# Performance work log

Hardware: AMD Instinct MI355X
Metric: run time of the kernel (lower is better)

Reference implementation:

```python
import jax, jax.numpy as jnp
import numpy as np

K = 3      # kernel size (fixed by 18 = 2*K*K offset channels)
PAD = 1
EPS = 1e-5 # BatchNorm eps


def setup_inputs() -> dict:
    key = jax.random.key(0)
    ks = jax.random.split(key, 4)
    B, Cin, Cout, H, W = 8, 64, 64, 96, 96
    x = jax.random.normal(ks[0], (B, Cin, H, W), jnp.float32)
    # small offset-conv weights so predicted offsets stay within a few pixels
    w_off = jax.random.normal(ks[1], (2 * K * K, Cin, K, K), jnp.float32) * 0.02
    b_off = jnp.zeros((2 * K * K,), jnp.float32)
    w_def = jax.random.normal(ks[2], (Cout, Cin, K, K), jnp.float32) * (1.0 / np.sqrt(Cin * K * K))
    b_def = jnp.zeros((Cout,), jnp.float32)
    gamma = jnp.ones((Cout,), jnp.float32)
    beta = jnp.zeros((Cout,), jnp.float32)
    return dict(x=x, w_off=w_off, b_off=b_off, w_def=w_def, b_def=b_def, gamma=gamma, beta=beta)


def _deform_sample(x, offset):
    """Bilinear-sample x at deformed kernel tap locations.
    x: (B,C,H,W); offset: (B,2*K*K,H,W) with (dy,dx) pairs per tap, row-major.
    Returns (B,C,K*K,H,W). Out-of-bounds samples are zero (torchvision semantics).
    """
    B, C, H, W = x.shape
    off = offset.reshape(B, K * K, 2, H, W)
    dy, dx = off[:, :, 0], off[:, :, 1]              # (B,9,H,W)
    ky = (jnp.arange(K * K) // K).astype(x.dtype)    # tap row index
    kx = (jnp.arange(K * K) % K).astype(x.dtype)     # tap col index
    base_y = jnp.arange(H, dtype=x.dtype)[:, None] - PAD   # (H,1)
    base_x = jnp.arange(W, dtype=x.dtype)[None, :] - PAD   # (1,W)
    py = dy + ky[None, :, None, None] + base_y[None, None]  # (B,9,H,W)
    px = dx + kx[None, :, None, None] + base_x[None, None]
    y0 = jnp.floor(py)
    x0 = jnp.floor(px)
    wy1 = py - y0
    wx1 = px - x0
    wy0 = 1.0 - wy1
    wx0 = 1.0 - wx1
    xflat = x.reshape(B, C, H * W)
    acc = jnp.zeros((B, C, K * K * H * W), x.dtype)
    corners = [(y0, x0, wy0 * wx0), (y0, x0 + 1.0, wy0 * wx1),
               (y0 + 1.0, x0, wy1 * wx0), (y0 + 1.0, x0 + 1.0, wy1 * wx1)]
    for yc, xc, wc in corners:
        valid = (yc >= 0) & (yc <= H - 1) & (xc >= 0) & (xc <= W - 1)
        iy = jnp.clip(yc, 0, H - 1).astype(jnp.int32)
        ix = jnp.clip(xc, 0, W - 1).astype(jnp.int32)
        idx = (iy * W + ix).reshape(B, 1, K * K * H * W)
        v = jnp.take_along_axis(xflat, idx, axis=2)          # (B,C,9HW) gather
        w = jnp.where(valid, wc, 0.0).reshape(B, 1, K * K * H * W)
        acc = acc + v * w
    return acc.reshape(B, C, K * K, H, W)


def reference(x, w_off, b_off, w_def, b_def, gamma, beta):
    # 1) offset-predicting conv
    offset = jax.lax.conv_general_dilated(
        x, w_off, window_strides=(1, 1), padding=((PAD, PAD), (PAD, PAD)),
        dimension_numbers=("NCHW", "OIHW", "NCHW")) + b_off[None, :, None, None]
    # 2) deformable conv: bilinear gather then per-pixel contraction over (C, taps)
    sampled = _deform_sample(x, offset)                      # (B,C,9,H,W)
    Cout = w_def.shape[0]
    y = jnp.einsum("bckhw,ock->bohw", sampled, w_def.reshape(Cout, -1, K * K))
    y = y + b_def[None, :, None, None]
    # 3) BatchNorm2d (training mode: batch statistics) + ReLU
    mean = y.mean(axis=(0, 2, 3))
    var = y.var(axis=(0, 2, 3))
    y = (y - mean[None, :, None, None]) * jax.lax.rsqrt(var[None, :, None, None] + EPS)
    y = gamma[None, :, None, None] * y + beta[None, :, None, None]
    return jax.nn.relu(y)
```

## Files before the change

### kernel.cpp

```cpp
#include <hip/hip_runtime.h>
#include <hip/hip_bf16.h>
#include <stdint.h>

static constexpr int NBATCH = 8;
static constexpr int Cin  = 64;
static constexpr int Cout = 64;
static constexpr int H = 96, W = 96;
static constexpr int HW   = H * W;
static constexpr int NPIX = NBATCH * HW;
static constexpr int NBLK = NPIX / 64;
static constexpr int BLK_PER_BATCH = HW / 64;
static constexpr float EPS = 1e-5f;

typedef short  bf16x8 __attribute__((ext_vector_type(8)));
typedef float  f32x4  __attribute__((ext_vector_type(4)));

__device__ inline uint16_t f2bf(float f) {
    __hip_bfloat16 h = __float2bfloat16(f);
    return *reinterpret_cast<uint16_t*>(&h);
}
__device__ inline float bf2f(uint16_t u) {
    union { uint32_t i; float f; } z;
    z.i = ((uint32_t)u) << 16;
    return z.f;
}

__global__ void repack(const float* __restrict__ w_off,
                       const float* __restrict__ w_def,
                       uint16_t* __restrict__ woffPack,
                       uint16_t* __restrict__ wdefPack) {
    int t0 = blockIdx.x * blockDim.x + threadIdx.x;
    int stride = gridDim.x * blockDim.x;
    for (int i = t0; i < 72 * 32 * 8; i += stride) {
        int e = i & 7;
        int n = (i >> 3) & 31;
        int sg = i >> 8;
        int k = sg * 8 + e;
        int tap = k >> 6, c = k & 63;
        woffPack[i] = (n < 18) ? f2bf(w_off[(n * Cin + c) * 9 + tap]) : (uint16_t)0;
    }
    for (int i = t0; i < 72 * 64 * 8; i += stride) {
        int e = i & 7;
        int n = (i >> 3) & 63;
        int sg = i >> 9;
        int k = sg * 8 + e;
        int tap = k >> 6, c = k & 63;
        wdefPack[i] = f2bf(w_def[(n * Cin + c) * 9 + tap]);
    }
}

__global__ __launch_bounds__(256) void transpose_x(const float* __restrict__ x,
                                                   uint16_t* __restrict__ xT) {
    int t = blockIdx.x * 256 + threadIdx.x;
    int pix  = t >> 1;
    int half = t & 1;
    int b = pix / HW, rem = pix % HW;
    const float* xb = x + (size_t)(b * Cin) * HW + rem + (size_t)(half * 32) * HW;
    uint16_t* o = xT + (size_t)pix * 64 + half * 32;
#pragma unroll
    for (int cg = 0; cg < 4; ++cg) {
        bf16x8 v;
#pragma unroll
        for (int e = 0; e < 8; ++e) v[e] = (short)f2bf(xb[(cg * 8 + e) * HW]);
        *reinterpret_cast<bf16x8*>(o + cg * 8) = v;
    }
}

__global__ __launch_bounds__(512, 4) void fused_deform(
        const uint16_t* __restrict__ xT,
        const uint16_t* __restrict__ woffPack,
        const uint16_t* __restrict__ wdefPack,
        const float* __restrict__ b_off,
        float* __restrict__ y,
        float* __restrict__ partial) {
    __shared__ __attribute__((aligned(16))) char smem[73728];
    __shared__ float offs[64 * 18];
    __shared__ float s_red[128];
    short* As   = (short*)smem;
    float* osum = (float*)smem;
    float* red  = (float*)smem;

    int tid  = threadIdx.x;
    int lane = tid & 63;
    int wv   = tid >> 6;
    int l15  = lane & 15;
    int lg   = lane >> 4;

    int wgid  = (blockIdx.x & 7) * BLK_PER_BATCH + (blockIdx.x >> 3);
    int gpix0 = wgid * 64;
    int b     = gpix0 / HW;
    int rem0  = gpix0 % HW;
    const uint16_t* xTb = xT + (size_t)b * HW * 64;

    int pr   = (wv << 3) + (lane >> 3);
    int e8   = lane & 7;
    int slot = e8 ^ (pr & 7);
    int remP = rem0 + pr;
    int hP   = remP / W, wP = remP % W;

#pragma unroll
    for (int tap = 0; tap < 9; ++tap) {
        int yy = hP + tap / 3 - 1;
        int xx = wP + tap % 3 - 1;
        bf16x8 v = (bf16x8){0, 0, 0, 0, 0, 0, 0, 0};
        if (yy >= 0 && yy < H && xx >= 0 && xx < W)
            v = *reinterpret_cast<const bf16x8*>(xTb + (yy * W + xx) * 64 + e8 * 8);
        *reinterpret_cast<bf16x8*>(&As[((tap * 64 + pr) * 8 + slot) * 8]) = v;
    }
    __syncthreads();

    {
        int wj = wv & 1;
        int kq = wv >> 1;
        int sbeg = (kq < 2) ? kq * 5 : 2 + kq * 4;
        int send = (kq < 2) ? sbeg + 5 : sbeg + 4;
        f32x4 oacc[4];
#pragma unroll
        for (int m = 0; m < 4; ++m) oacc[m] = (f32x4){0.f, 0.f, 0.f, 0.f};
        for (int s = sbeg; s < send; ++s) {
            int sg = s * 4 + lg;
            bf16x8 bb = *reinterpret_cast<const bf16x8*>(
                woffPack + (sg * 32 + wj * 16 + l15) * 8);
#pragma unroll
            for (int m = 0; m < 4; ++m) {
                bf16x8 a = *reinterpret_cast<const bf16x8*>(
                    &As[(((sg >> 3) * 64 + m * 16 + l15) * 8 + ((sg & 7) ^ (l15 & 7))) * 8]);
                oacc[m] = __builtin_amdgcn_mfma_f32_16x16x32_bf16(a, bb, oacc[m], 0, 0, 0);
            }
        }
        __syncthreads();
#pragma unroll
        for (int m = 0; m < 4; ++m)
#pragma unroll
            for (int r = 0; r < 4; ++r)
                osum[(kq * 64 + m * 16 + lg * 4 + r) * 34 + wj * 16 + l15] = oacc[m][r];
        __syncthreads();
        for (int i = tid; i < 64 * 18; i += 512) {
            int rr = i / 18, o = i - rr * 18;
            offs[i] = osum[rr * 34 + o] + osum[(64 + rr) * 34 + o]
                    + osum[(128 + rr) * 34 + o] + osum[(192 + rr) * 34 + o] + b_off[o];
        }
        if (tid < 128) s_red[tid] = 0.f;
        __syncthreads();
    }

    float hm1 = (float)(hP - 1), wm1 = (float)(wP - 1);
#pragma unroll
    for (int tap = 0; tap < 9; ++tap) {
        float dy = offs[pr * 18 + 2 * tap];
        float dx = offs[pr * 18 + 2 * tap + 1];
        float py = dy + (float)(tap / 3) + hm1;
        float px = dx + (float)(tap % 3) + wm1;
        float y0f = floorf(py), x0f = floorf(px);
        float wy1 = py - y0f, wx1 = px - x0f;
        float wy0 = 1.f - wy1, wx0 = 1.f - wx1;
        int iy0 = (int)y0f, ix0 = (int)x0f;
        int iy1 = iy0 + 1,  ix1 = ix0 + 1;
        bool vy0 = (iy0 >= 0) && (iy0 < H), vy1 = (iy1 >= 0) && (iy1 < H);
        bool vx0 = (ix0 >= 0) && (ix0 < W), vx1 = (ix1 >= 0) && (ix1 < W);
        float w00 = (vy0 && vx0) ? wy0 * wx0 : 0.f;
        float w01 = (vy0 && vx1) ? wy0 * wx1 : 0.f;
        float w10 = (vy1 && vx0) ? wy1 * wx0 : 0.f;
        float w11 = (vy1 && vx1) ? wy1 * wx1 : 0.f;
        int cy0 = min(max(iy0, 0), H - 1), cy1 = min(max(iy1, 0), H - 1);
        int cx0 = min(max(ix0, 0), W - 1), cx1 = min(max(ix1, 0), W - 1);
        const uint16_t* basep = xTb + e8 * 8;
        bf16x8 v00 = *reinterpret_cast<const bf16x8*>(basep + (cy0 * W + cx0) * 64);
        bf16x8 v01 = *reinterpret_cast<const bf16x8*>(basep + (cy0 * W + cx1) * 64);
        bf16x8 v10 = *reinterpret_cast<const bf16x8*>(basep + (cy1 * W + cx0) * 64);
        bf16x8 v11 = *reinterpret_cast<const bf16x8*>(basep + (cy1 * W + cx1) * 64);
        bf16x8 outv;
#pragma unroll
        for (int e = 0; e < 8; ++e) {
            float s = w00 * bf2f((uint16_t)v00[e]) + w01 * bf2f((uint16_t)v01[e])
                    + w10 * bf2f((uint16_t)v10[e]) + w11 * bf2f((uint16_t)v11[e]);
            outv[e] = (short)f2bf(s);
        }
        *reinterpret_cast<bf16x8*>(&As[((tap * 64 + pr) * 8 + slot) * 8]) = outv;
    }
    __syncthreads();

    {
        int nf = wv & 3;
        int kh = wv >> 2;
        f32x4 acc[4];
#pragma unroll
        for (int m = 0; m < 4; ++m) acc[m] = (f32x4){0.f, 0.f, 0.f, 0.f};
#pragma unroll
        for (int s = 0; s < 9; ++s) {
            int sg = (kh * 9 + s) * 4 + lg;
            bf16x8 bb = *reinterpret_cast<const bf16x8*>(
                wdefPack + (sg * 64 + nf * 16 + l15) * 8);
#pragma unroll
            for (int m = 0; m < 4; ++m) {
                bf16x8 a = *reinterpret_cast<const bf16x8*>(
                    &As[(((sg >> 3) * 64 + m * 16 + l15) * 8 + ((sg & 7) ^ (l15 & 7))) * 8]);
                acc[m] = __builtin_amdgcn_mfma_f32_16x16x32_bf16(a, bb, acc[m], 0, 0, 0);
            }
        }
        __syncthreads();
#pragma unroll
        for (int m = 0; m < 4; ++m)
#pragma unroll
            for (int r = 0; r < 4; ++r)
                red[(kh * 64 + m * 16 + lg * 4 + r) * 66 + nf * 16 + l15] = acc[m][r];
        __syncthreads();

        int c  = lane;
        int rg = wv;
        f32x4 v0, v1;
        float s = 0.f, q = 0.f;
#pragma unroll
        for (int k2 = 0; k2 < 8; ++k2) {
            int r = rg * 8 + k2;
            float v = red[r * 66 + c] + red[(64 + r) * 66 + c];
            if (k2 < 4) v0[k2] = v; else v1[k2 - 4] = v;
            s += v; q += v * v;
        }
        float* yp = y + ((size_t)b * Cout + c) * HW + rem0 + rg * 8;
        *reinterpret_cast<f32x4*>(yp)     = v0;
        *reinterpret_cast<f32x4*>(yp + 4) = v1;
        atomicAdd(&s_red[c], s);
        atomicAdd(&s_red[64 + c], q);
    }
    __syncthreads();
    if (tid < 128) partial[(size_t)wgid * 128 + tid] = s_red[tid];
}

__global__ __launch_bounds__(256) void bn_reduce1(const float* __restrict__ partial,
                                                  float* __restrict__ partial2) {
    __shared__ float red[256];
    int ch = threadIdx.x & 127;
    int g  = threadIdx.x >> 7;
    float s = 0.f;
#pragma unroll
    for (int r = 0; r < 8; ++r)
        s += partial[(size_t)(blockIdx.x * 16 + g * 8 + r) * 128 + ch];
    red[threadIdx.x] = s;
    __syncthreads();
    if (g == 0)
        partial2[(size_t)blockIdx.x * 128 + ch] = red[ch] + red[128 + ch];
}

__global__ void bn_stats2(const float* __restrict__ partial2,
                          const float* __restrict__ gamma,
                          const float* __restrict__ beta,
                          float* __restrict__ stats) {
    __shared__ float red[256];
    int ch = threadIdx.x & 127;
    int g  = threadIdx.x >> 7;
    float s = 0.f;
    for (int i = 0; i < 36; ++i)
        s += partial2[(size_t)(g * 36 + i) * 128 + ch];
    red[threadIdx.x] = s;
    __syncthreads();
    if (threadIdx.x < 64) {
        int c = threadIdx.x;
        float sum = red[c] + red[128 + c];
        float sq  = red[64 + c] + red[192 + c];
        float mean = sum / (float)NPIX;
        float var  = sq / (float)NPIX - mean * mean;
        float v    = var + EPS;
        float inv  = rsqrtf(v);
        inv = inv * (1.5f - 0.5f * v * inv * inv);
        float sc = gamma[c] * inv;
        stats[c]      = sc;
        stats[64 + c] = beta[c] - mean * sc;
    }
}

__global__ __launch_bounds__(256) void bn_apply(float* __restrict__ y,
                                                const float* __restrict__ stats) {
    int t = blockIdx.x * blockDim.x + threadIdx.x;
    int e = t * 4;
    int ch = (e / HW) % Cout;
    float sc = stats[ch];
    float sh = stats[64 + ch];
    float4 v = *reinterpret_cast<float4*>(y + e);
    v.x = fmaxf(v.x * sc + sh, 0.f);
    v.y = fmaxf(v.y * sc + sh, 0.f);
    v.z = fmaxf(v.z * sc + sh, 0.f);
    v.w = fmaxf(v.w * sc + sh, 0.f);
    *reinterpret_cast<float4*>(y + e) = v;
}

extern "C" void kernel_launch(void* const* d_in, const int* in_sizes, int n_in,
                              void* d_out, int out_size, void* d_ws, size_t ws_size,
                              hipStream_t stream) {
    const float* x     = (const float*)d_in[0];
    const float* w_off = (const float*)d_in[1];
    const float* b_off = (const float*)d_in[2];
    const float* w_def = (const float*)d_in[3];
    const float* gamma = (const float*)d_in[5];
    const float* beta  = (const float*)d_in[6];
    float* out = (float*)d_out;
    char*  ws  = (char*)d_ws;

    uint16_t* xT       = (uint16_t*)ws;
    uint16_t* woffPack = (uint16_t*)(ws + 9437184);
    uint16_t* wdefPack = (uint16_t*)(ws + 9474048);
    float*    partial  = (float*)(ws + 9547776);
    float*    partial2 = (float*)(ws + 10137600);
    float*    stats    = (float*)(ws + 10174464);

    repack<<<64, 256, 0, stream>>>(w_off, w_def, woffPack, wdefPack);
    transpose_x<<<NPIX * 2 / 256, 256, 0, stream>>>(x, xT);
    fused_deform<<<NBLK, 512, 0, stream>>>(xT, woffPack, wdefPack, b_off,
                                           out, partial);
    bn_reduce1<<<72, 256, 0, stream>>>(partial, partial2);
    bn_stats2<<<1, 256, 0, stream>>>(partial2, gamma, beta, stats);
    bn_apply<<<(NPIX * Cout / 4) / 256, 256, 0, stream>>>(out, stats);
}
```

Before: 69.26 us.

## Halve pixel tile to 32 and read offset-conv operands directly from global

Shrinks the per-workgroup pixel tile from 64 to 32, which halves LDS use and doubles the workgroup count, and raises the launch-bounds occupancy hint from 4 to 8. The offset conv no longer stages the 9-tap im2col in LDS. It loads A fragments straight from the transposed input in global memory with bounds masking, which removes one staging pass and one barrier. Bilinear sampling is re-split so the two halves of the block handle different tap ranges, and the BN partial reduction is resized for the doubled number of partials. The cost is more redundant global loads, since neighbouring tiles overlap more and the weight fragments are fetched once per smaller tile.

```diff
diff --git a/kernel.cpp b/kernel.cpp
--- a/kernel.cpp
+++ b/kernel.cpp
@@ -8,8 +8,9 @@
 static constexpr int H = 96, W = 96;
 static constexpr int HW   = H * W;
 static constexpr int NPIX = NBATCH * HW;
-static constexpr int NBLK = NPIX / 64;
-static constexpr int BLK_PER_BATCH = HW / 64;
+static constexpr int NTILE = 32;
+static constexpr int NBLK = NPIX / NTILE;
+static constexpr int BLK_PER_BATCH = HW / NTILE;
 static constexpr float EPS = 1e-5f;
 
 typedef short  bf16x8 __attribute__((ext_vector_type(8)));
@@ -66,15 +67,15 @@
     }
 }
 
-__global__ __launch_bounds__(512, 4) void fused_deform(
+__global__ __launch_bounds__(512, 8) void fused_deform(
         const uint16_t* __restrict__ xT,
         const uint16_t* __restrict__ woffPack,
         const uint16_t* __restrict__ wdefPack,
         const float* __restrict__ b_off,
         float* __restrict__ y,
         float* __restrict__ partial) {
-    __shared__ __attribute__((aligned(16))) char smem[73728];
-    __shared__ float offs[64 * 18];
+    __shared__ __attribute__((aligned(16))) char smem[36864];
+    __shared__ float offs[NTILE * 18];
     __shared__ float s_red[128];
     short* As   = (short*)smem;
     float* osum = (float*)smem;
@@ -87,139 +88,135 @@
     int lg   = lane >> 4;
 
     int wgid  = (blockIdx.x & 7) * BLK_PER_BATCH + (blockIdx.x >> 3);
-    int gpix0 = wgid * 64;
+    int gpix0 = wgid * NTILE;
     int b     = gpix0 / HW;
     int rem0  = gpix0 % HW;
+    int h0    = rem0 / W;
+    int w0    = rem0 % W;
     const uint16_t* xTb = xT + (size_t)b * HW * 64;
 
-    int pr   = (wv << 3) + (lane >> 3);
-    int e8   = lane & 7;
-    int slot = e8 ^ (pr & 7);
-    int remP = rem0 + pr;
-    int hP   = remP / W, wP = remP % W;
-
-#pragma unroll
-    for (int tap = 0; tap < 9; ++tap) {
-        int yy = hP + tap / 3 - 1;
-        int xx = wP + tap % 3 - 1;
-        bf16x8 v = (bf16x8){0, 0, 0, 0, 0, 0, 0, 0};
-        if (yy >= 0 && yy < H && xx >= 0 && xx < W)
-            v = *reinterpret_cast<const bf16x8*>(xTb + (yy * W + xx) * 64 + e8 * 8);
-        *reinterpret_cast<bf16x8*>(&As[((tap * 64 + pr) * 8 + slot) * 8]) = v;
-    }
-    __syncthreads();
+    if (tid < 128) s_red[tid] = 0.f;
 
     {
         int wj = wv & 1;
         int kq = wv >> 1;
         int sbeg = (kq < 2) ? kq * 5 : 2 + kq * 4;
         int send = (kq < 2) ? sbeg + 5 : sbeg + 4;
-        f32x4 oacc[4];
-#pragma unroll
-        for (int m = 0; m < 4; ++m) oacc[m] = (f32x4){0.f, 0.f, 0.f, 0.f};
+        f32x4 oacc[2];
+        oacc[0] = (f32x4){0.f, 0.f, 0.f, 0.f};
+        oacc[1] = (f32x4){0.f, 0.f, 0.f, 0.f};
         for (int s = sbeg; s < send; ++s) {
             int sg = s * 4 + lg;
+            int tap = sg >> 3, ch = sg & 7;
+            int ty = tap / 3, tx = tap % 3;
+            int yy = h0 + ty - 1;
             bf16x8 bb = *reinterpret_cast<const bf16x8*>(
                 woffPack + (sg * 32 + wj * 16 + l15) * 8);
 #pragma unroll
-            for (int m = 0; m < 4; ++m) {
+            for (int m = 0; m < 2; ++m) {
+                int xx = w0 + m * 16 + l15 + tx - 1;
+                bool ok = (yy >= 0) && (yy < H) && (xx >= 0) && (xx < W);
+                int cy = min(max(yy, 0), H - 1);
+                int cx = min(max(xx, 0), W - 1);
                 bf16x8 a = *reinterpret_cast<const bf16x8*>(
-                    &As[(((sg >> 3) * 64 + m * 16 + l15) * 8 + ((sg & 7) ^ (l15 & 7))) * 8]);
+                    xTb + (cy * W + cx) * 64 + ch * 8);
+                if (!ok) a = (bf16x8){0, 0, 0, 0, 0, 0, 0, 0};
                 oacc[m] = __builtin_amdgcn_mfma_f32_16x16x32_bf16(a, bb, oacc[m], 0, 0, 0);
             }
         }
+#pragma unroll
+        for (int m = 0; m < 2; ++m)
+#pragma unroll
+            for (int r = 0; r < 4; ++r)
+                osum[(kq * 32 + m * 16 + lg * 4 + r) * 34 + wj * 16 + l15] = oacc[m][r];
         __syncthreads();
-#pragma unroll
-        for (int m = 0; m < 4; ++m)
-#pragma unroll
-            for (int r = 0; r < 4; ++r)
-                osum[(kq * 64 + m * 16 + lg * 4 + r) * 34 + wj * 16 + l15] = oacc[m][r];
+        for (int i = tid; i < NTILE * 18; i += 512) {
+            int rr = i / 18, o = i - rr * 18;
+            offs[i] = osum[rr * 34 + o] + osum[(32 + rr) * 34 + o]
+                    + osum[(64 + rr) * 34 + o] + osum[(96 + rr) * 34 + o] + b_off[o];
+        }
         __syncthreads();
-        for (int i = tid; i < 64 * 18; i += 512) {
-            int rr = i / 18, o = i - rr * 18;
-            offs[i] = osum[rr * 34 + o] + osum[(64 + rr) * 34 + o]
-                    + osum[(128 + rr) * 34 + o] + osum[(192 + rr) * 34 + o] + b_off[o];
-        }
-        if (tid < 128) s_red[tid] = 0.f;
-        __syncthreads();
-    }
-
-    float hm1 = (float)(hP - 1), wm1 = (float)(wP - 1);
-#pragma unroll
-    for (int tap = 0; tap < 9; ++tap) {
-        float dy = offs[pr * 18 + 2 * tap];
-        float dx = offs[pr * 18 + 2 * tap + 1];
-        float py = dy + (float)(tap / 3) + hm1;
-        float px = dx + (float)(tap % 3) + wm1;
-        float y0f = floorf(py), x0f = floorf(px);
-        float wy1 = py - y0f, wx1 = px - x0f;
-        float wy0 = 1.f - wy1, wx0 = 1.f - wx1;
-        int iy0 = (int)y0f, ix0 = (int)x0f;
-        int iy1 = iy0 + 1,  ix1 = ix0 + 1;
-        bool vy0 = (iy0 >= 0) && (iy0 < H), vy1 = (iy1 >= 0) && (iy1 < H);
-        bool vx0 = (ix0 >= 0) && (ix0 < W), vx1 = (ix1 >= 0) && (ix1 < W);
-        float w00 = (vy0 && vx0) ? wy0 * wx0 : 0.f;
-        float w01 = (vy0 && vx1) ? wy0 * wx1 : 0.f;
-        float w10 = (vy1 && vx0) ? wy1 * wx0 : 0.f;
-        float w11 = (vy1 && vx1) ? wy1 * wx1 : 0.f;
-        int cy0 = min(max(iy0, 0), H - 1), cy1 = min(max(iy1, 0), H - 1);
-        int cx0 = min(max(ix0, 0), W - 1), cx1 = min(max(ix1, 0), W - 1);
-        const uint16_t* basep = xTb + e8 * 8;
-        bf16x8 v00 = *reinterpret_cast<const bf16x8*>(basep + (cy0 * W + cx0) * 64);
-        bf16x8 v01 = *reinterpret_cast<const bf16x8*>(basep + (cy0 * W + cx1) * 64);
-        bf16x8 v10 = *reinterpret_cast<const bf16x8*>(basep + (cy1 * W + cx0) * 64);
-        bf16x8 v11 = *reinterpret_cast<const bf16x8*>(basep + (cy1 * W + cx1) * 64);
-        bf16x8 outv;
-#pragma unroll
-        for (int e = 0; e < 8; ++e) {
-            float s = w00 * bf2f((uint16_t)v00[e]) + w01 * bf2f((uint16_t)v01[e])
-                    + w10 * bf2f((uint16_t)v10[e]) + w11 * bf2f((uint16_t)v11[e]);
-            outv[e] = (short)f2bf(s);
-        }
-        *reinterpret_cast<bf16x8*>(&As[((tap * 64 + pr) * 8 + slot) * 8]) = outv;
+    }
+
+    {
+        int e8 = tid & 7;
+        int pr = (tid >> 3) & 31;
+        int g  = tid >> 8;
+        int slot = e8 ^ (pr & 7);
+        float hm1 = (float)(h0 - 1), wm1 = (float)(w0 + pr - 1);
+        int tbeg = g ? 5 : 0, tend = g ? 9 : 5;
+        for (int tap = tbeg; tap < tend; ++tap) {
+            float dy = offs[pr * 18 + 2 * tap];
+            float dx = offs[pr * 18 + 2 * tap + 1];
+            float py = dy + (float)(tap / 3) + hm1;
+            float px = dx + (float)(tap % 3) + wm1;
+            float y0f = floorf(py), x0f = floorf(px);
+            float wy1 = py - y0f, wx1 = px - x0f;
+            float wy0 = 1.f - wy1, wx0 = 1.f - wx1;
+            int iy0 = (int)y0f, ix0 = (int)x0f;
+            int iy1 = iy0 + 1,  ix1 = ix0 + 1;
+            bool vy0 = (iy0 >= 0) && (iy0 < H), vy1 = (iy1 >= 0) && (iy1 < H);
+            bool vx0 = (ix0 >= 0) && (ix0 < W), vx1 = (ix1 >= 0) && (ix1 < W);
+            float w00 = (vy0 && vx0) ? wy0 * wx0 : 0.f;
+            float w01 = (vy0 && vx1) ? wy0 * wx1 : 0.f;
+            float w10 = (vy1 && vx0) ? wy1 * wx0 : 0.f;
+            float w11 = (vy1 && vx1) ? wy1 * wx1 : 0.f;
+            int cy0 = min(max(iy0, 0), H - 1), cy1 = min(max(iy1, 0), H - 1);
+            int cx0 = min(max(ix0, 0), W - 1), cx1 = min(max(ix1, 0), W - 1);
+            const uint16_t* basep = xTb + e8 * 8;
+            bf16x8 v00 = *reinterpret_cast<const bf16x8*>(basep + (cy0 * W + cx0) * 64);
+            bf16x8 v01 = *reinterpret_cast<const bf16x8*>(basep + (cy0 * W + cx1) * 64);
+            bf16x8 v10 = *reinterpret_cast<const bf16x8*>(basep + (cy1 * W + cx0) * 64);
+            bf16x8 v11 = *reinterpret_cast<const bf16x8*>(basep + (cy1 * W + cx1) * 64);
+            bf16x8 outv;
+#pragma unroll
+            for (int e = 0; e < 8; ++e) {
+                float s = w00 * bf2f((uint16_t)v00[e]) + w01 * bf2f((uint16_t)v01[e])
+                        + w10 * bf2f((uint16_t)v10[e]) + w11 * bf2f((uint16_t)v11[e]);
+                outv[e] = (short)f2bf(s);
+            }
+            *reinterpret_cast<bf16x8*>(&As[((tap * 32 + pr) * 8 + slot) * 8]) = outv;
+        }
     }
     __syncthreads();
 
     {
         int nf = wv & 3;
         int kh = wv >> 2;
-        f32x4 acc[4];
-#pragma unroll
-        for (int m = 0; m < 4; ++m) acc[m] = (f32x4){0.f, 0.f, 0.f, 0.f};
-#pragma unroll
+        f32x4 acc[2];
+        acc[0] = (f32x4){0.f, 0.f, 0.f, 0.f};
+        acc[1] = (f32x4){0.f, 0.f, 0.f, 0.f};
+#pragma unroll 3
         for (int s = 0; s < 9; ++s) {
             int sg = (kh * 9 + s) * 4 + lg;
             bf16x8 bb = *reinterpret_cast<const bf16x8*>(
                 wdefPack + (sg * 64 + nf * 16 + l15) * 8);
 #pragma unroll
-            for (int m = 0; m < 4; ++m) {
+            for (int m = 0; m < 2; ++m) {
                 bf16x8 a = *reinterpret_cast<const bf16x8*>(
-                    &As[(((sg >> 3) * 64 + m * 16 + l15) * 8 + ((sg & 7) ^ (l15 & 7))) * 8]);
+                    &As[(((sg >> 3) * 32 + m * 16 + l15) * 8 + ((sg & 7) ^ (l15 & 7))) * 8]);
                 acc[m] = __builtin_amdgcn_mfma_f32_16x16x32_bf16(a, bb, acc[m], 0, 0, 0);
             }
         }
         __syncthreads();
 #pragma unroll
-        for (int m = 0; m < 4; ++m)
+        for (int m = 0; m < 2; ++m)
 #pragma unroll
             for (int r = 0; r < 4; ++r)
-                red[(kh * 64 + m * 16 + lg * 4 + r) * 66 + nf * 16 + l15] = acc[m][r];
+                red[(kh * 32 + m * 16 + lg * 4 + r) * 66 + nf * 16 + l15] = acc[m][r];
         __syncthreads();
 
-        int c  = lane;
-        int rg = wv;
-        f32x4 v0, v1;
+        int c    = tid >> 3;
+        int pgrp = (tid & 7) * 4;
         float s = 0.f, q = 0.f;
-#pragma unroll
-        for (int k2 = 0; k2 < 8; ++k2) {
-            int r = rg * 8 + k2;
-            float v = red[r * 66 + c] + red[(64 + r) * 66 + c];
-            if (k2 < 4) v0[k2] = v; else v1[k2 - 4] = v;
-            s += v; q += v * v;
-        }
-        float* yp = y + ((size_t)b * Cout + c) * HW + rem0 + rg * 8;
-        *reinterpret_cast<f32x4*>(yp)     = v0;
-        *reinterpret_cast<f32x4*>(yp + 4) = v1;
+        f32x4 v;
+#pragma unroll
+        for (int i = 0; i < 4; ++i) {
+            int r = pgrp + i;
+            float val = red[r * 66 + c] + red[(32 + r) * 66 + c];
+            v[i] = val; s += val; q += val * val;
+        }
+        *reinterpret_cast<f32x4*>(y + ((size_t)b * Cout + c) * HW + rem0 + pgrp) = v;
         atomicAdd(&s_red[c], s);
         atomicAdd(&s_red[64 + c], q);
     }
@@ -234,8 +231,8 @@
     int g  = threadIdx.x >> 7;
     float s = 0.f;
 #pragma unroll
-    for (int r = 0; r < 8; ++r)
-        s += partial[(size_t)(blockIdx.x * 16 + g * 8 + r) * 128 + ch];
+    for (int r = 0; r < 16; ++r)
+        s += partial[(size_t)(blockIdx.x * 32 + g * 16 + r) * 128 + ch];
     red[threadIdx.x] = s;
     __syncthreads();
     if (g == 0)
@@ -300,8 +297,8 @@
     uint16_t* woffPack = (uint16_t*)(ws + 9437184);
     uint16_t* wdefPack = (uint16_t*)(ws + 9474048);
     float*    partial  = (float*)(ws + 9547776);
-    float*    partial2 = (float*)(ws + 10137600);
-    float*    stats    = (float*)(ws + 10174464);
+    float*    partial2 = (float*)(ws + 10727424);
+    float*    stats    = (float*)(ws + 10764288);
 
     repack<<<64, 256, 0, stream>>>(w_off, w_def, woffPack, wdefPack);
     transpose_x<<<NPIX * 2 / 256, 256, 0, stream>>>(x, xT);
```

Result: slower. 77.82 us (+12.3%).

## Stage im2col taps via global_load_lds and share bilinear setup across lanes

Applied to the files above, without the earlier changes.

The initial 3x3 neighbourhood load into LDS now uses direct global-to-LDS 16-byte loads, with out-of-bounds taps redirected to a zeroed scratch page written by the repack kernel. The swizzled slot is applied on the global source side so the LDS layout stays the same as before. In the deformable sampling stage, each of the 8 lanes that share a pixel computes the bilinear weights and indices for one tap, and the values are broadcast with shuffles, so the per-tap scalar math is no longer repeated across all 8 lanes. Tap 8 is still computed redundantly. The aim is to cut VGPR traffic and redundant ALU work, at the cost of 8 shuffles per tap and a dependence on the global_load_lds layout matching the previous LDS indexing.

```diff
diff --git a/kernel.cpp b/kernel.cpp
--- a/kernel.cpp
+++ b/kernel.cpp
@@ -24,13 +24,20 @@
     z.i = ((uint32_t)u) << 16;
     return z.f;
 }
+__device__ inline void gld_lds16(const void* g, void* l) {
+    __builtin_amdgcn_global_load_lds(
+        (const __attribute__((address_space(1))) void*)g,
+        (__attribute__((address_space(3))) void*)l, 16, 0, 0);
+}
 
 __global__ void repack(const float* __restrict__ w_off,
                        const float* __restrict__ w_def,
                        uint16_t* __restrict__ woffPack,
-                       uint16_t* __restrict__ wdefPack) {
+                       uint16_t* __restrict__ wdefPack,
+                       float* __restrict__ zeropage) {
     int t0 = blockIdx.x * blockDim.x + threadIdx.x;
     int stride = gridDim.x * blockDim.x;
+    if (t0 < 64) zeropage[t0] = 0.f;
     for (int i = t0; i < 72 * 32 * 8; i += stride) {
         int e = i & 7;
         int n = (i >> 3) & 31;
@@ -71,6 +78,7 @@
         const uint16_t* __restrict__ woffPack,
         const uint16_t* __restrict__ wdefPack,
         const float* __restrict__ b_off,
+        const float* __restrict__ zeropage,
         float* __restrict__ y,
         float* __restrict__ partial) {
     __shared__ __attribute__((aligned(16))) char smem[73728];
@@ -98,14 +106,18 @@
     int remP = rem0 + pr;
     int hP   = remP / W, wP = remP % W;
 
-#pragma unroll
-    for (int tap = 0; tap < 9; ++tap) {
-        int yy = hP + tap / 3 - 1;
-        int xx = wP + tap % 3 - 1;
-        bf16x8 v = (bf16x8){0, 0, 0, 0, 0, 0, 0, 0};
-        if (yy >= 0 && yy < H && xx >= 0 && xx < W)
-            v = *reinterpret_cast<const bf16x8*>(xTb + (yy * W + xx) * 64 + e8 * 8);
-        *reinterpret_cast<bf16x8*>(&As[((tap * 64 + pr) * 8 + slot) * 8]) = v;
+    {
+        const uint16_t* gsrc = xTb + slot * 8;
+        char* ldsbase = (char*)As + (size_t)wv * 1024;
+#pragma unroll
+        for (int tap = 0; tap < 9; ++tap) {
+            int yy = hP + tap / 3 - 1;
+            int xx = wP + tap % 3 - 1;
+            bool ok = (yy >= 0) && (yy < H) && (xx >= 0) && (xx < W);
+            const void* g = ok ? (const void*)(gsrc + (yy * W + xx) * 64)
+                               : (const void*)zeropage;
+            gld_lds16(g, ldsbase + tap * 8192);
+        }
     }
     __syncthreads();
 
@@ -144,39 +156,84 @@
         __syncthreads();
     }
 
-    float hm1 = (float)(hP - 1), wm1 = (float)(wP - 1);
-#pragma unroll
-    for (int tap = 0; tap < 9; ++tap) {
-        float dy = offs[pr * 18 + 2 * tap];
-        float dx = offs[pr * 18 + 2 * tap + 1];
-        float py = dy + (float)(tap / 3) + hm1;
-        float px = dx + (float)(tap % 3) + wm1;
-        float y0f = floorf(py), x0f = floorf(px);
-        float wy1 = py - y0f, wx1 = px - x0f;
-        float wy0 = 1.f - wy1, wx0 = 1.f - wx1;
-        int iy0 = (int)y0f, ix0 = (int)x0f;
-        int iy1 = iy0 + 1,  ix1 = ix0 + 1;
-        bool vy0 = (iy0 >= 0) && (iy0 < H), vy1 = (iy1 >= 0) && (iy1 < H);
-        bool vx0 = (ix0 >= 0) && (ix0 < W), vx1 = (ix1 >= 0) && (ix1 < W);
-        float w00 = (vy0 && vx0) ? wy0 * wx0 : 0.f;
-        float w01 = (vy0 && vx1) ? wy0 * wx1 : 0.f;
-        float w10 = (vy1 && vx0) ? wy1 * wx0 : 0.f;
-        float w11 = (vy1 && vx1) ? wy1 * wx1 : 0.f;
-        int cy0 = min(max(iy0, 0), H - 1), cy1 = min(max(iy1, 0), H - 1);
-        int cx0 = min(max(ix0, 0), W - 1), cx1 = min(max(ix1, 0), W - 1);
+    {
+        float hm1 = (float)(hP - 1), wm1 = (float)(wP - 1);
+        float w00a, w01a, w10a, w11a; int i00a, i01a, i10a, i11a;
+        {
+            int t = e8;
+            int ty = (t * 11) >> 5;
+            int tx = t - 3 * ty;
+            float dy = offs[pr * 18 + 2 * t];
+            float dx = offs[pr * 18 + 2 * t + 1];
+            float py = dy + (float)ty + hm1;
+            float px = dx + (float)tx + wm1;
+            float y0f = floorf(py), x0f = floorf(px);
+            float wy1 = py - y0f, wx1 = px - x0f;
+            float wy0 = 1.f - wy1, wx0 = 1.f - wx1;
+            int iy0 = (int)y0f, ix0 = (int)x0f;
+            int iy1 = iy0 + 1,  ix1 = ix0 + 1;
+            bool vy0 = (iy0 >= 0) && (iy0 < H), vy1 = (iy1 >= 0) && (iy1 < H);
+            bool vx0 = (ix0 >= 0) && (ix0 < W), vx1 = (ix1 >= 0) && (ix1 < W);
+            w00a = (vy0 && vx0) ? wy0 * wx0 : 0.f;
+            w01a = (vy0 && vx1) ? wy0 * wx1 : 0.f;
+            w10a = (vy1 && vx0) ? wy1 * wx0 : 0.f;
+            w11a = (vy1 && vx1) ? wy1 * wx1 : 0.f;
+            int cy0 = min(max(iy0, 0), H - 1), cy1 = min(max(iy1, 0), H - 1);
+            int cx0 = min(max(ix0, 0), W - 1), cx1 = min(max(ix1, 0), W - 1);
+            i00a = cy0 * W + cx0; i01a = cy0 * W + cx1;
+            i10a = cy1 * W + cx0; i11a = cy1 * W + cx1;
+        }
+        float w00b, w01b, w10b, w11b; int i00b, i01b, i10b, i11b;
+        {
+            float dy = offs[pr * 18 + 16];
+            float dx = offs[pr * 18 + 17];
+            float py = dy + 2.f + hm1;
+            float px = dx + 2.f + wm1;
+            float y0f = floorf(py), x0f = floorf(px);
+            float wy1 = py - y0f, wx1 = px - x0f;
+            float wy0 = 1.f - wy1, wx0 = 1.f - wx1;
+            int iy0 = (int)y0f, ix0 = (int)x0f;
+            int iy1 = iy0 + 1,  ix1 = ix0 + 1;
+            bool vy0 = (iy0 >= 0) && (iy0 < H), vy1 = (iy1 >= 0) && (iy1 < H);
+            bool vx0 = (ix0 >= 0) && (ix0 < W), vx1 = (ix1 >= 0) && (ix1 < W);
+            w00b = (vy0 && vx0) ? wy0 * wx0 : 0.f;
+            w01b = (vy0 && vx1) ? wy0 * wx1 : 0.f;
+            w10b = (vy1 && vx0) ? wy1 * wx0 : 0.f;
+            w11b = (vy1 && vx1) ? wy1 * wx1 : 0.f;
+            int cy0 = min(max(iy0, 0), H - 1), cy1 = min(max(iy1, 0), H - 1);
+            int cx0 = min(max(ix0, 0), W - 1), cx1 = min(max(ix1, 0), W - 1);
+            i00b = cy0 * W + cx0; i01b = cy0 * W + cx1;
+            i10b = cy1 * W + cx0; i11b = cy1 * W + cx1;
+        }
+
         const uint16_t* basep = xTb + e8 * 8;
-        bf16x8 v00 = *reinterpret_cast<const bf16x8*>(basep + (cy0 * W + cx0) * 64);
-        bf16x8 v01 = *reinterpret_cast<const bf16x8*>(basep + (cy0 * W + cx1) * 64);
-        bf16x8 v10 = *reinterpret_cast<const bf16x8*>(basep + (cy1 * W + cx0) * 64);
-        bf16x8 v11 = *reinterpret_cast<const bf16x8*>(basep + (cy1 * W + cx1) * 64);
-        bf16x8 outv;
-#pragma unroll
-        for (int e = 0; e < 8; ++e) {
-            float s = w00 * bf2f((uint16_t)v00[e]) + w01 * bf2f((uint16_t)v01[e])
-                    + w10 * bf2f((uint16_t)v10[e]) + w11 * bf2f((uint16_t)v11[e]);
-            outv[e] = (short)f2bf(s);
-        }
-        *reinterpret_cast<bf16x8*>(&As[((tap * 64 + pr) * 8 + slot) * 8]) = outv;
+        int lanebase = lane & 56;
+#pragma unroll
+        for (int tap = 0; tap < 9; ++tap) {
+            float w00, w01, w10, w11; int i00, i01, i10, i11;
+            if (tap < 8) {
+                int src = lanebase + tap;
+                w00 = __shfl(w00a, src); w01 = __shfl(w01a, src);
+                w10 = __shfl(w10a, src); w11 = __shfl(w11a, src);
+                i00 = __shfl(i00a, src); i01 = __shfl(i01a, src);
+                i10 = __shfl(i10a, src); i11 = __shfl(i11a, src);
+            } else {
+                w00 = w00b; w01 = w01b; w10 = w10b; w11 = w11b;
+                i00 = i00b; i01 = i01b; i10 = i10b; i11 = i11b;
+            }
+            bf16x8 v00 = *reinterpret_cast<const bf16x8*>(basep + i00 * 64);
+            bf16x8 v01 = *reinterpret_cast<const bf16x8*>(basep + i01 * 64);
+            bf16x8 v10 = *reinterpret_cast<const bf16x8*>(basep + i10 * 64);
+            bf16x8 v11 = *reinterpret_cast<const bf16x8*>(basep + i11 * 64);
+            bf16x8 outv;
+#pragma unroll
+            for (int e = 0; e < 8; ++e) {
+                float s = w00 * bf2f((uint16_t)v00[e]) + w01 * bf2f((uint16_t)v01[e])
+                        + w10 * bf2f((uint16_t)v10[e]) + w11 * bf2f((uint16_t)v11[e]);
+                outv[e] = (short)f2bf(s);
+            }
+            *reinterpret_cast<bf16x8*>(&As[((tap * 64 + pr) * 8 + slot) * 8]) = outv;
+        }
     }
     __syncthreads();
 
@@ -302,11 +359,12 @@
     float*    partial  = (float*)(ws + 9547776);
     float*    partial2 = (float*)(ws + 10137600);
     float*    stats    = (float*)(ws + 10174464);
-
-    repack<<<64, 256, 0, stream>>>(w_off, w_def, woffPack, wdefPack);
+    float*    zeropage = (float*)(ws + 10174976);
+
+    repack<<<64, 256, 0, stream>>>(w_off, w_def, woffPack, wdefPack, zeropage);
     transpose_x<<<NPIX * 2 / 256, 256, 0, stream>>>(x, xT);
     fused_deform<<<NBLK, 512, 0, stream>>>(xT, woffPack, wdefPack, b_off,
-                                           out, partial);
+                                           zeropage, out, partial);
     bn_reduce1<<<72, 256, 0, stream>>>(partial, partial2);
     bn_stats2<<<1, 256, 0, stream>>>(partial2, gamma, beta, stats);
     bn_apply<<<(NPIX * Cout / 4) / 256, 256, 0, stream>>>(out, stats);
```

Measured after the change: 67.08 us. 1.03x faster.
